# Optimization experiments

Measured on AMD Instinct MI355X. Metric: run time of the kernel, lower is better.

The kernel has to match this reference:

```python
import jax, jax.numpy as jnp
import numpy as np

B, C, F, D = 128, 16, 128, 512


def setup_inputs() -> dict:
    key = jax.random.key(0)
    k1, k2 = jax.random.split(key)
    return {
        "c_feats": jax.random.normal(k1, (B, C, D), dtype=jnp.float32),
        "f_feats": jax.random.normal(k2, (B, F, D), dtype=jnp.float32),
    }


def _dtw_path_masks(S):
    """S: [P, c, f] per-pair similarity. Returns [P, c, f] 0/1 max-path masks.

    DP: D[i,j] = max(D[i-1,j], D[i,j-1], D[i-1,j-1]) + S[i-1,j-1], D[0,0]=0,
    borders -inf. Tie-break priority (up, left, diag) matches Python max().
    Row recurrence is vectorized: D[i,j] = Csum[j] + cummax_k<=j(A[k]-Csum[k-1])
    where A[k]=max(D[i-1,k], D[i-1,k-1]) (wavefront-free row-parallel form).
    """
    P_, c, f = S.shape
    NEG = -jnp.inf

    init = jnp.concatenate([jnp.zeros((P_, 1), S.dtype),
                            jnp.full((P_, f), NEG, S.dtype)], axis=1)  # D[0, 0..f]

    def row_step(prev, dt_row):
        # prev: [P, f+1] = D[i-1, 0..f]; dt_row: [P, f] = S[i-1, :]
        A = jnp.maximum(prev[:, 1:], prev[:, :-1])                  # max(D[i-1,j], D[i-1,j-1])
        Ccum = jnp.cumsum(dt_row, axis=1)
        Cm1 = jnp.concatenate([jnp.zeros((P_, 1), dt_row.dtype), Ccum[:, :-1]], axis=1)
        row = Ccum + jax.lax.cummax(A - Cm1, axis=1)                # D[i, 1..f]
        new_prev = jnp.concatenate([jnp.full((P_, 1), NEG, dt_row.dtype), row], axis=1)
        return new_prev, new_prev

    _, rows = jax.lax.scan(row_step, init, jnp.moveaxis(S, 1, 0))   # [c, P, f+1]
    Dm = jnp.moveaxis(jnp.concatenate([init[None], rows], axis=0), 1, 0)  # [P, c+1, f+1]

    # Predecessor choice per cell; argmax picks first max -> priority up,left,diag
    up = Dm[:, :-1, 1:]
    left = Dm[:, 1:, :-1]
    diag = Dm[:, :-1, :-1]
    mv = jnp.argmax(jnp.stack([up, left, diag], axis=-1), axis=-1).astype(jnp.int32)
    mv = jnp.pad(mv, ((0, 0), (1, 0), (1, 0)))                      # [P, c+1, f+1]

    pidx = jnp.arange(P_)

    def bt_step(carry, _):
        mask, i, j = carry
        active = (i > 0) | (j > 0)
        mask = mask.at[pidx, i - 1, j - 1].add(jnp.where(active, 1.0, 0.0).astype(mask.dtype))
        m = mv[pidx, i, j]
        di = jnp.where(m == 1, 0, 1)   # left keeps i
        dj = jnp.where(m == 0, 0, 1)   # up keeps j
        i = jnp.where(active, i - di, i)
        j = jnp.where(active, j - dj, j)
        return (mask, i, j), None

    mask0 = jnp.zeros((P_, c, f), jnp.float32)
    i0 = jnp.full((P_,), c, jnp.int32)
    j0 = jnp.full((P_,), f, jnp.int32)
    (mask, _, _), _ = jax.lax.scan(bt_step, (mask0, i0, j0), None, length=c + f)
    return mask


def reference(c_feats, f_feats):
    b, c, d = c_feats.shape
    f = f_feats.shape[1]
    xn = c_feats / jnp.linalg.norm(c_feats, axis=-1, keepdims=True)
    yn = f_feats / jnp.linalg.norm(f_feats, axis=-1, keepdims=True)
    # Source quirk: y row j is normalized only once outer index i reaches it
    # (y[i-1] bug), so S[i,j] uses normalized y[j] iff j <= i, raw y[j] otherwise.
    Sn = jnp.einsum('mcd,nfd->mncf', xn, yn)
    Sr = jnp.einsum('mcd,nfd->mncf', xn, f_feats)
    tri = jnp.arange(f)[None, :] <= jnp.arange(c)[:, None]          # [c, f]: j <= i
    S = jnp.where(tri, Sn, Sr).reshape(b * b, c, f)
    return _dtw_path_masks(S).reshape(b, b, c, f)
```

## Files before the change

kernel.cpp:

```cpp
#include <hip/hip_runtime.h>
#include <stdint.h>

#define M_TOT 2048
#define N_TOT 16384
#define K_TOT 512

typedef _Float16 f16x8 __attribute__((ext_vector_type(8)));
typedef float f32x4 __attribute__((ext_vector_type(4)));
typedef float f32x16 __attribute__((ext_vector_type(16)));

#define AS1 __attribute__((address_space(1)))
#define AS3 __attribute__((address_space(3)))

__device__ __forceinline__ void ld_lds16(const void* g, void* l) {
    __builtin_amdgcn_global_load_lds((const AS1 void*)g, (AS3 void*)l, 16, 0, 0);
}

__device__ __forceinline__ void split4(float x0, float x1, float x2, float x3,
                                       uint2* hs, uint2* ls) {
    union U { _Float16 h[4]; uint2 u; } H, L;
    _Float16 h0 = (_Float16)x0; H.h[0] = h0; L.h[0] = (_Float16)(x0 - (float)h0);
    _Float16 h1 = (_Float16)x1; H.h[1] = h1; L.h[1] = (_Float16)(x1 - (float)h1);
    _Float16 h2 = (_Float16)x2; H.h[2] = h2; L.h[2] = (_Float16)(x2 - (float)h2);
    _Float16 h3 = (_Float16)x3; H.h[3] = h3; L.h[3] = (_Float16)(x3 - (float)h3);
    *hs = H.u; *ls = L.u;
}

__global__ __launch_bounds__(256) void norm_split_kernel(
    const float* __restrict__ c_feats, const float* __restrict__ f_feats,
    _Float16* __restrict__ Ah, _Float16* __restrict__ Al,
    _Float16* __restrict__ Bh, _Float16* __restrict__ Bl,
    float* __restrict__ normf)
{
    int wave = blockIdx.x * 4 + (threadIdx.x >> 6);
    int lane = threadIdx.x & 63;
    if (wave < 2048) {
        const float* row = c_feats + (size_t)wave * K_TOT;
        float4 v0 = ((const float4*)row)[lane];
        float4 v1 = ((const float4*)row)[lane + 64];
        double ss = (double)v0.x * v0.x + (double)v0.y * v0.y +
                    (double)v0.z * v0.z + (double)v0.w * v0.w +
                    (double)v1.x * v1.x + (double)v1.y * v1.y +
                    (double)v1.z * v1.z + (double)v1.w * v1.w;
        #pragma unroll
        for (int off = 32; off; off >>= 1) ss += __shfl_down(ss, off);
        double tot = __shfl(ss, 0);
        float nrm = sqrtf((float)tot);
        float a0 = v0.x / nrm, a1 = v0.y / nrm, a2 = v0.z / nrm, a3 = v0.w / nrm;
        float b0 = v1.x / nrm, b1 = v1.y / nrm, b2 = v1.z / nrm, b3 = v1.w / nrm;
        uint2 h, l;
        split4(a0, a1, a2, a3, &h, &l);
        ((uint2*)(Ah + (size_t)wave * K_TOT))[lane] = h;
        ((uint2*)(Al + (size_t)wave * K_TOT))[lane] = l;
        split4(b0, b1, b2, b3, &h, &l);
        ((uint2*)(Ah + (size_t)wave * K_TOT))[lane + 64] = h;
        ((uint2*)(Al + (size_t)wave * K_TOT))[lane + 64] = l;
    } else if (wave < 18432) {
        int fr = wave - 2048;
        const float* row = f_feats + (size_t)fr * K_TOT;
        float4 v0 = ((const float4*)row)[lane];
        float4 v1 = ((const float4*)row)[lane + 64];
        double ss = (double)v0.x * v0.x + (double)v0.y * v0.y +
                    (double)v0.z * v0.z + (double)v0.w * v0.w +
                    (double)v1.x * v1.x + (double)v1.y * v1.y +
                    (double)v1.z * v1.z + (double)v1.w * v1.w;
        #pragma unroll
        for (int off = 32; off; off >>= 1) ss += __shfl_down(ss, off);
        if (lane == 0) normf[fr] = sqrtf((float)ss);
        uint2 h, l;
        split4(v0.x, v0.y, v0.z, v0.w, &h, &l);
        ((uint2*)(Bh + (size_t)fr * K_TOT))[lane] = h;
        ((uint2*)(Bl + (size_t)fr * K_TOT))[lane] = l;
        split4(v1.x, v1.y, v1.z, v1.w, &h, &l);
        ((uint2*)(Bh + (size_t)fr * K_TOT))[lane + 64] = h;
        ((uint2*)(Bl + (size_t)fr * K_TOT))[lane + 64] = l;
    }
}

__global__ __launch_bounds__(256, 2) void mfma_gemm_kernel(
    const _Float16* __restrict__ Ah, const _Float16* __restrict__ Al,
    const _Float16* __restrict__ Bh, const _Float16* __restrict__ Bl,
    const float* __restrict__ normf,
    float* __restrict__ out)
{
    __shared__ _Float16 sAh[128 * 32];
    __shared__ _Float16 sAl[128 * 32];
    __shared__ _Float16 sBh[128 * 32];
    __shared__ _Float16 sBl[128 * 32];

    const int t = threadIdx.x;
    const int w = t >> 6, lane = t & 63;
    const int gm0 = blockIdx.y * 128, gn0 = blockIdx.x * 128;
    const int wm = (w & 1) * 64, wn = (w >> 1) * 64;
    const int m32 = lane & 31, ko8 = (lane >> 5) * 8;

    f32x16 acc[2][2] = {};
    const int l0 = w * 128 + lane;

    for (int k0 = 0; k0 < K_TOT; k0 += 32) {
        #pragma unroll
        for (int c = 0; c < 2; ++c) {
            int l = l0 + c * 64;
            int row = l >> 2, kq = l & 3;
            size_t goffA = (size_t)(gm0 + row) * K_TOT + k0 + kq * 8;
            size_t goffB = (size_t)(gn0 + row) * K_TOT + k0 + kq * 8;
            ld_lds16(Ah + goffA, sAh + (size_t)l * 8);
            ld_lds16(Al + goffA, sAl + (size_t)l * 8);
            ld_lds16(Bh + goffB, sBh + (size_t)l * 8);
            ld_lds16(Bl + goffB, sBl + (size_t)l * 8);
        }
        __syncthreads();

        #pragma unroll
        for (int kh = 0; kh < 2; ++kh) {
            f16x8 fah[2], fal[2], fbh[2], fbl[2];
            #pragma unroll
            for (int x = 0; x < 2; ++x) {
                int ar = (wm + x * 32 + m32) * 32 + kh * 16 + ko8;
                int br = (wn + x * 32 + m32) * 32 + kh * 16 + ko8;
                fah[x] = *(const f16x8*)(sAh + ar);
                fal[x] = *(const f16x8*)(sAl + ar);
                fbh[x] = *(const f16x8*)(sBh + br);
                fbl[x] = *(const f16x8*)(sBl + br);
            }
            #pragma unroll
            for (int mi = 0; mi < 2; ++mi)
                #pragma unroll
                for (int ni = 0; ni < 2; ++ni) {
                    acc[mi][ni] = __builtin_amdgcn_mfma_f32_32x32x16_f16(fah[mi], fbl[ni], acc[mi][ni], 0, 0, 0);
                    acc[mi][ni] = __builtin_amdgcn_mfma_f32_32x32x16_f16(fal[mi], fbh[ni], acc[mi][ni], 0, 0, 0);
                    acc[mi][ni] = __builtin_amdgcn_mfma_f32_32x32x16_f16(fah[mi], fbh[ni], acc[mi][ni], 0, 0, 0);
                }
        }
        __syncthreads();
    }

    const int nn = blockIdx.x;
    const int rq = 4 * (lane >> 5);
    #pragma unroll
    for (int ni = 0; ni < 2; ++ni) {
        int col = wn + ni * 32 + m32;
        bool cn = (col < 16);
        float nf = cn ? normf[gn0 + col] : 1.f;
        #pragma unroll
        for (int mi = 0; mi < 2; ++mi) {
            #pragma unroll
            for (int reg = 0; reg < 16; ++reg) {
                int r = wm + mi * 32 + (reg & 3) + 8 * (reg >> 2) + rq;
                int gm = gm0 + r;
                int mm = gm >> 4, ii = gm & 15;
                float v = acc[mi][ni][reg];
                if (cn && col <= ii) v /= nf;
                out[(((size_t)mm * 128 + nn) * 16 + ii) * 128 + col] = v;
            }
        }
    }
}

__global__ __launch_bounds__(256) void dtw_kernel(float* __restrict__ buf)
{
    __shared__ uint8_t mv_lds[4][4][2064];
    __shared__ int bounds[4][4][16];

    const int lane = threadIdx.x & 63;
    const int w = threadIdx.x >> 6;
    const int q = lane >> 4, r = lane & 15;
    const int pbase = blockIdx.x * 16 + w * 4;
    const int p = pbase + q;
    float* tile = buf + (size_t)p * 2048;
    const float4* row4 = (const float4*)(tile + r * 128);
    uint8_t* mymv = &mv_lds[w][q][0];

    const double NEG = -1e300;
    double Dp = NEG, Dp2 = NEG;
    float4 cur4 = {0, 0, 0, 0};
    float4 nxt4 = row4[0];

    for (int t = 0; t < 143; ++t) {
        int j = t - r;
        bool act = (j >= 0) & (j < 128);
        if (act & ((j & 3) == 0)) {
            cur4 = nxt4;
            if (j + 4 < 128) nxt4 = row4[(j >> 2) + 1];
        }
        int e = j & 3;
        float sv = (e == 0) ? cur4.x : (e == 1) ? cur4.y : (e == 2) ? cur4.z : cur4.w;
        double up = __shfl_up(Dp, 1);
        double dg = __shfl_up(Dp2, 1);
        double lf = Dp;
        if (r == 0) up = NEG;
        if (j == 0) {
            lf = NEG;
            dg = (r == 0) ? 0.0 : NEG;
        } else if (r == 0) {
            dg = NEG;
        }
        int m = (up >= lf && up >= dg) ? 0 : ((lf >= dg) ? 1 : 2);
        double Dc = fmax(up, fmax(lf, dg)) + (double)sv;
        if (act) mymv[j * 16 + r] = (uint8_t)m;
        Dp2 = Dp;
        Dp = Dc;
    }
    __syncthreads();

    if (r == 0) {
        int i = 16, jj = 128, hic = 127;
        for (int it = 0; it < 160; ++it) {
            if (i <= 0) break;
            int m = mymv[(jj - 1) * 16 + (i - 1)];
            if (m == 1) { --jj; continue; }
            bounds[w][q][i - 1] = (jj - 1) | (hic << 8);
            if (m == 2) --jj;
            --i;
            hic = jj - 1;
        }
    }
    __syncthreads();

    #pragma unroll 4
    for (int it = 0; it < 32; ++it) {
        int flat = it * 64 + lane;
        int q2 = flat >> 9;
        int rem = flat & 511;
        int ii = rem >> 5;
        int c4 = rem & 31;
        int b = bounds[w][q2][ii];
        int lo = b & 0xff, hi = (b >> 8) & 0xff;
        int j0 = c4 * 4;
        float4 v;
        v.x = (j0 + 0 >= lo && j0 + 0 <= hi) ? 1.f : 0.f;
        v.y = (j0 + 1 >= lo && j0 + 1 <= hi) ? 1.f : 0.f;
        v.z = (j0 + 2 >= lo && j0 + 2 <= hi) ? 1.f : 0.f;
        v.w = (j0 + 3 >= lo && j0 + 3 <= hi) ? 1.f : 0.f;
        float* tb = buf + (size_t)(pbase + q2) * 2048;
        *(float4*)(tb + ii * 128 + j0) = v;
    }
}

extern "C" void kernel_launch(void* const* d_in, const int* in_sizes, int n_in,
                              void* d_out, int out_size, void* d_ws, size_t ws_size,
                              hipStream_t stream)
{
    const float* c_feats = (const float*)d_in[0];
    const float* f_feats = (const float*)d_in[1];
    float* out = (float*)d_out;

    _Float16* Ah = (_Float16*)d_ws;
    _Float16* Al = Ah + (size_t)M_TOT * K_TOT;
    _Float16* Bh = Al + (size_t)M_TOT * K_TOT;
    _Float16* Bl = Bh + (size_t)N_TOT * K_TOT;
    float* normf = (float*)(Bl + (size_t)N_TOT * K_TOT);

    norm_split_kernel<<<4608, 256, 0, stream>>>(c_feats, f_feats, Ah, Al, Bh, Bl, normf);
    dim3 g(N_TOT / 128, M_TOT / 128);
    mfma_gemm_kernel<<<g, 256, 0, stream>>>(Ah, Al, Bh, Bl, normf, out);
    dtw_kernel<<<1024, 256, 0, stream>>>(out);
}
```

Before: 365.1 us.

## Swizzle GEMM LDS tiles and pack DTW move bits to cut LDS

The GEMM kernel now XOR-swizzles the 16-byte k-chunk index by row bits, both when staging tiles through global_load_lds and when reading MFMA fragments. This is meant to reduce LDS bank conflicts on fragment reads. The DTW kernel packs its 2-bit predecessor moves into 32-bit words, dropping the per-cell byte array. That shrinks LDS use so the new launch bound of 8 blocks per CU can hold, and cuts the number of LDS stores, at the cost of a little bit-manipulation in the DP loop and the backtrace.

```diff
diff --git a/kernel.cpp b/kernel.cpp
--- a/kernel.cpp
+++ b/kernel.cpp
@@ -92,7 +92,8 @@
     const int w = t >> 6, lane = t & 63;
     const int gm0 = blockIdx.y * 128, gn0 = blockIdx.x * 128;
     const int wm = (w & 1) * 64, wn = (w >> 1) * 64;
-    const int m32 = lane & 31, ko8 = (lane >> 5) * 8;
+    const int m32 = lane & 31;
+    const int kql0 = lane >> 5;
 
     f32x16 acc[2][2] = {};
     const int l0 = w * 128 + lane;
@@ -101,9 +102,10 @@
         #pragma unroll
         for (int c = 0; c < 2; ++c) {
             int l = l0 + c * 64;
-            int row = l >> 2, kq = l & 3;
-            size_t goffA = (size_t)(gm0 + row) * K_TOT + k0 + kq * 8;
-            size_t goffB = (size_t)(gn0 + row) * K_TOT + k0 + kq * 8;
+            int lrow = l >> 2, kq = l & 3;
+            int kqs = kq ^ ((lrow >> 1) & 3);
+            size_t goffA = (size_t)(gm0 + lrow) * K_TOT + k0 + kqs * 8;
+            size_t goffB = (size_t)(gn0 + lrow) * K_TOT + k0 + kqs * 8;
             ld_lds16(Ah + goffA, sAh + (size_t)l * 8);
             ld_lds16(Al + goffA, sAl + (size_t)l * 8);
             ld_lds16(Bh + goffB, sBh + (size_t)l * 8);
@@ -116,8 +118,12 @@
             f16x8 fah[2], fal[2], fbh[2], fbl[2];
             #pragma unroll
             for (int x = 0; x < 2; ++x) {
-                int ar = (wm + x * 32 + m32) * 32 + kh * 16 + ko8;
-                int br = (wn + x * 32 + m32) * 32 + kh * 16 + ko8;
+                int arr = wm + x * 32 + m32;
+                int brr = wn + x * 32 + m32;
+                int kqa = (kh * 2 + kql0) ^ ((arr >> 1) & 3);
+                int kqb = (kh * 2 + kql0) ^ ((brr >> 1) & 3);
+                int ar = arr * 32 + kqa * 8;
+                int br = brr * 32 + kqb * 8;
                 fah[x] = *(const f16x8*)(sAh + ar);
                 fal[x] = *(const f16x8*)(sAl + ar);
                 fbh[x] = *(const f16x8*)(sBh + br);
@@ -157,9 +163,9 @@
     }
 }
 
-__global__ __launch_bounds__(256) void dtw_kernel(float* __restrict__ buf)
-{
-    __shared__ uint8_t mv_lds[4][4][2064];
+__global__ __launch_bounds__(256, 8) void dtw_kernel(float* __restrict__ buf)
+{
+    __shared__ uint32_t mvw[4][4][132];
     __shared__ int bounds[4][4][16];
 
     const int lane = threadIdx.x & 63;
@@ -169,12 +175,13 @@
     const int p = pbase + q;
     float* tile = buf + (size_t)p * 2048;
     const float4* row4 = (const float4*)(tile + r * 128);
-    uint8_t* mymv = &mv_lds[w][q][0];
+    uint32_t* mvq = &mvw[w][q][0];
 
     const double NEG = -1e300;
     double Dp = NEG, Dp2 = NEG;
     float4 cur4 = {0, 0, 0, 0};
     float4 nxt4 = row4[0];
+    uint32_t mvbuf = 0;
 
     for (int t = 0; t < 143; ++t) {
         int j = t - r;
@@ -197,7 +204,13 @@
         }
         int m = (up >= lf && up >= dg) ? 0 : ((lf >= dg) ? 1 : 2);
         double Dc = fmax(up, fmax(lf, dg)) + (double)sv;
-        if (act) mymv[j * 16 + r] = (uint8_t)m;
+        if (act) {
+            mvbuf |= (uint32_t)m << (2 * (j & 15));
+            if ((j & 15) == 15) {
+                mvq[r * 8 + (j >> 4)] = mvbuf;
+                mvbuf = 0;
+            }
+        }
         Dp2 = Dp;
         Dp = Dc;
     }
@@ -207,7 +220,8 @@
         int i = 16, jj = 128, hic = 127;
         for (int it = 0; it < 160; ++it) {
             if (i <= 0) break;
-            int m = mymv[(jj - 1) * 16 + (i - 1)];
+            uint32_t word = mvq[(i - 1) * 8 + ((jj - 1) >> 4)];
+            int m = (int)((word >> (2 * ((jj - 1) & 15))) & 3u);
             if (m == 1) { --jj; continue; }
             bounds[w][q][i - 1] = (jj - 1) | (hic << 8);
             if (m == 2) --jj;
```

New measurement: 371.2 us. Within noise of the previous version (+1.7%).
